# Kernel optimization log

Hardware: AMD Instinct MI355X
Metric: run time of the kernel (lower is better)

## Reference

```python
import jax, jax.numpy as jnp
import numpy as np

# GNB per-element parameters [s, beta, R, C6] indexed by atomic number Z (rows not listed stay zero)
_ROWS = {
 1:[0.2772,1.7504,3.6516,95.99], 2:[0.2425,2.087,2.1843,40.67], 3:[0.3266,2.3073,1.2711,70.21],
 4:[0.3964,2.8811,3.3497,114.51], 5:[0.3121,2.6366,2.7079,152.36], 6:[0.2455,3.0189,1.8219,184.28],
 7:[0.2743,2.9432,2.4667,482.54], 8:[0.2577,2.7407,2.365,405.57], 9:[0.2791,2.5863,1.5062,218.45],
 10:[0.2378,2.5307,1.8233,174.81], 11:[0.2592,2.5679,1.3974,181.7], 12:[0.3837,2.9613,3.3515,263.02],
 13:[0.3013,3.2377,3.0102,228.1], 14:[0.3202,3.2749,3.1629,359.43], 15:[0.3399,3.7491,3.2554,3222.12],
 16:[0.3215,3.6718,2.9539,2144.49], 17:[0.3071,3.418,3.0368,2072.46], 18:[0.2752,3.3306,2.6598,1357.42],
 19:[0.2264,2.9736,4.0877,1406.65], 20:[0.4015,3.4464,4.1275,1058.36], 21:[0.9388,4.5955,9.7282,11498.73],
 22:[0.6048,3.5334,8.5322,3361.33], 23:[0.3678,3.068,7.2344,2095.91], 24:[0.2848,2.8393,5.3605,1049.31],
 25:[0.355,3.055,3.718,966.27], 26:[0.4406,3.2628,3.6408,1571.36], 27:[0.4124,3.2622,3.4961,1183.59],
 28:[0.3139,2.749,3.5108,787.76], 29:[0.3345,2.9097,3.0537,563.93], 30:[0.3391,2.9024,3.0261,592.91],
 31:[0.3146,3.3924,3.1735,430.82], 32:[0.3327,3.2804,3.1773,812.57], 33:[0.404,3.8757,3.8357,4533.53],
 34:[0.3343,3.8562,3.1109,3440.92], 35:[0.3242,3.7067,3.2122,3859.82], 36:[0.292,3.6457,2.8263,2729.6],
 37:[0.2677,3.4421,2.412,1864.19], 38:[0.3446,3.559,1.894,1175.73], 39:[1.0038,5.7293,11.2061,32141.18],
 40:[0.6146,5.075,6.821,27655.14], 41:[0.4244,3.7156,7.2367,2864.2], 42:[0.4882,3.6853,3.901,3563.45],
 43:[0.4439,3.6987,4.0857,3266.43], 44:[0.4736,3.7826,4.045,3967.23], 45:[0.4039,3.4706,3.4813,2233.82],
 46:[0.3188,3.3433,3.0487,1393.49], 47:[0.2948,3.1186,2.7795,1315.09], 48:[0.3012,3.0853,2.8673,1311.47],
 49:[0.3351,3.5452,3.3339,1460.56], 50:[0.3134,3.2997,3.0086,1662.99], 51:[0.4081,4.1277,3.9919,8089.97],
 52:[0.3585,4.1795,3.4209,6887.05], 53:[0.3574,4.0988,3.5649,8799.32], 54:[0.3134,4.0387,3.0288,6136.5],
 55:[0.2872,3.8468,2.262,3757.31], 56:[0.3788,4.0368,1.3837,2561.18], 57:[1.0851,6.1365,12.171,66580.83],
 72:[0.5577,5.213,6.0791,27593.76], 73:[0.5308,4.7637,5.7661,15364.65], 74:[0.3926,3.6018,3.6366,2734.5],
 75:[0.5351,3.9552,4.241,4801.82], 76:[0.4701,4.0278,4.1348,5685.94], 77:[0.3661,3.6123,3.4213,2786.0],
 78:[0.3411,3.6066,3.2486,2699.79], 79:[0.3164,3.3822,2.9588,2282.6], 80:[0.3047,3.375,2.9381,2476.79],
 81:[0.2802,3.3964,2.7711,2988.7], 82:[0.2682,3.2481,2.5816,2506.63], 83:[0.3876,4.1225,3.785,8916.84],
 84:[0.3679,4.2313,3.5381,8694.22], 85:[0.368,4.2455,3.6985,11821.61], 86:[0.3195,4.1784,3.0551,8410.64],
}
_TAB = np.zeros((87, 4), np.float32)
for _z, _v in _ROWS.items():
    _TAB[_z] = _v
GNB_TABLE = jnp.asarray(_TAB)
C_SP2 = jnp.asarray(np.array([0.2808, 3.0548, 2.2348, 429.69], np.float32))
C_SP3 = jnp.asarray(np.array([0.2455, 3.0189, 1.8219, 184.28], np.float32))
N_CN2 = jnp.asarray(np.array([0.2996, 3.02, 2.6454, 720.18], np.float32))
N_CN3 = jnp.asarray(np.array([0.2743, 2.9432, 2.4667, 482.54], np.float32))

BJ_A1, BJ_A2, BJ_ALPHA = 0.4, 4.0, 14.0
CUTOFF_LR, CUTOFF_START = 10.0, 8.0  # cutoff_start = cutoff_lr - 2.0


def _poly_envelope(x):
    # PolynomialCutoff.calculate_envelope with r_max=1, p=6:
    x6 = x ** 6
    env = 1.0 - 28.0 * x6 + 48.0 * x6 * x - 21.0 * x6 * x * x
    return env * (x < 1.0)


def _gnb_forward(lengths, Z, edge_index):
    n_nodes = Z.shape[0]
    sender, receiver = edge_index[0], edge_index[1]

    # coordination numbers via scatter-add on receiver
    cn = jnp.zeros((n_nodes,), jnp.int32).at[receiver].add(1)

    # species-indexed params with CN-adaptive selection for C and N
    params = GNB_TABLE[Z]  # [N, 4]
    c_params = jnp.where((cn <= 3)[:, None], C_SP2[None, :], C_SP3[None, :])
    n_params = jnp.where((cn <= 2)[:, None], N_CN2[None, :], N_CN3[None, :])
    params = jnp.where((Z == 6)[:, None], c_params, params)
    params = jnp.where((Z == 7)[:, None], n_params, params)

    R_i = params[:, 2]
    C6_i = params[:, 3]

    # geometric-mean combination rules per edge
    C6_ij = jnp.sqrt(C6_i[sender] * C6_i[receiver])
    R_ij = jnp.sqrt(R_i[sender] * R_i[receiver])

    r = lengths
    # BJ damping: f = 1 / (1 + 6 (r/r0)^(-alpha)), r0 = a1 sqrt(R_ij) + a2
    r0 = BJ_A1 * jnp.sqrt(R_ij) + BJ_A2
    f_damp = 1.0 / (1.0 + 6.0 * (r0 / r) ** BJ_ALPHA)

    e_edge = -C6_ij / (R_ij ** 6 + r ** 6) * f_damp

    # long-range polynomial cutoff switching from 1 at cutoff_start to 0 at cutoff_lr
    x = (r - CUTOFF_START) / (CUTOFF_LR - CUTOFF_START)
    env = jnp.where(r < CUTOFF_START, 1.0, _poly_envelope(x))
    e_edge = e_edge * env

    # scatter-sum to atoms; 0.5 to split symmetric pair energy over both directions
    node_energy = jnp.zeros((n_nodes,), e_edge.dtype).at[receiver].add(0.5 * e_edge)
    return node_energy


def setup_inputs() -> dict:
    key = jax.random.key(0)
    k1, k2, k3 = jax.random.split(key, 3)
    n_nodes, n_edges = 100000, 6400000
    Z = jax.random.randint(k1, (n_nodes,), 1, 87, dtype=jnp.int32)
    edge_index = jax.random.randint(k2, (2, n_edges), 0, n_nodes, dtype=jnp.int32)
    lengths = jax.random.uniform(k3, (n_edges,), jnp.float32, 1.0, 10.5)
    return {"Z": Z, "edge_index": edge_index, "lengths": lengths}


def reference(Z, edge_index, lengths):
    return _gnb_forward(lengths, Z, edge_index)
```

## Files before the change

kernel.cpp:

```cpp
#include <hip/hip_runtime.h>


#define B2SHIFT 10
#define B2SIZE  1024
#define TILE    4096
#define SBLK    512
#define ESLICES 8
#define MAXB    128
#define EB      256
#define AREP    4

__device__ __constant__ float2 GNB_RC6[87] = {
    {0.f, 0.f},
    {3.6516f, 95.99f},   {2.1843f, 40.67f},   {1.2711f, 70.21f},
    {3.3497f, 114.51f},  {2.7079f, 152.36f},  {1.8219f, 184.28f},
    {2.4667f, 482.54f},  {2.365f, 405.57f},   {1.5062f, 218.45f},
    {1.8233f, 174.81f},  {1.3974f, 181.7f},   {3.3515f, 263.02f},
    {3.0102f, 228.1f},   {3.1629f, 359.43f},  {3.2554f, 3222.12f},
    {2.9539f, 2144.49f}, {3.0368f, 2072.46f}, {2.6598f, 1357.42f},
    {4.0877f, 1406.65f}, {4.1275f, 1058.36f}, {9.7282f, 11498.73f},
    {8.5322f, 3361.33f}, {7.2344f, 2095.91f}, {5.3605f, 1049.31f},
    {3.718f, 966.27f},   {3.6408f, 1571.36f}, {3.4961f, 1183.59f},
    {3.5108f, 787.76f},  {3.0537f, 563.93f},  {3.0261f, 592.91f},
    {3.1735f, 430.82f},  {3.1773f, 812.57f},  {3.8357f, 4533.53f},
    {3.1109f, 3440.92f}, {3.2122f, 3859.82f}, {2.8263f, 2729.6f},
    {2.412f, 1864.19f},  {1.894f, 1175.73f},  {11.2061f, 32141.18f},
    {6.821f, 27655.14f}, {7.2367f, 2864.2f},  {3.901f, 3563.45f},
    {4.0857f, 3266.43f}, {4.045f, 3967.23f},  {3.4813f, 2233.82f},
    {3.0487f, 1393.49f}, {2.7795f, 1315.09f}, {2.8673f, 1311.47f},
    {3.3339f, 1460.56f}, {3.0086f, 1662.99f}, {3.9919f, 8089.97f},
    {3.4209f, 6887.05f}, {3.5649f, 8799.32f}, {3.0288f, 6136.5f},
    {2.262f, 3757.31f},  {1.3837f, 2561.18f}, {12.171f, 66580.83f},
    {0.f,0.f},{0.f,0.f},{0.f,0.f},{0.f,0.f},{0.f,0.f},{0.f,0.f},{0.f,0.f},
    {0.f,0.f},{0.f,0.f},{0.f,0.f},{0.f,0.f},{0.f,0.f},{0.f,0.f},{0.f,0.f},
    {6.0791f, 27593.76f}, {5.7661f, 15364.65f}, {3.6366f, 2734.5f},
    {4.241f, 4801.82f},   {4.1348f, 5685.94f},  {3.4213f, 2786.0f},
    {3.2486f, 2699.79f},  {2.9588f, 2282.6f},   {2.9381f, 2476.79f},
    {2.7711f, 2988.7f},   {2.5816f, 2506.63f},  {3.785f, 8916.84f},
    {3.5381f, 8694.22f},  {3.6985f, 11821.61f}, {3.0551f, 8410.64f},
};

__global__ void gnb_init(const int* __restrict__ Z, unsigned* __restrict__ isCN,
                         int nw, int n_nodes, int4* __restrict__ zp4, int zq,
                         int* __restrict__ zp, int zwords) {
    int stride = gridDim.x * blockDim.x;
    int t0 = blockIdx.x * blockDim.x + threadIdx.x;
    int4 z4 = make_int4(0, 0, 0, 0);
    for (int i = t0; i < zq; i += stride) zp4[i] = z4;
    for (int i = zq * 4 + t0; i < zwords; i += stride) zp[i] = 0;
    for (int w = t0; w < nw; w += stride) {
        unsigned m = 0;
        int base = w << 5;
        int lim = n_nodes - base; if (lim > 32) lim = 32;
        for (int k = 0; k < lim; ++k) {
            int z = Z[base + k];
            if (z == 6 || z == 7) m |= (1u << k);
        }
        isCN[w] = m;
    }
}

__global__ void __launch_bounds__(EB)
gnb_degree(const int* __restrict__ recv, const unsigned* __restrict__ isCN,
           int* __restrict__ cn, int n_edges) {
    int base = (blockIdx.x * EB + threadIdx.x) * 4;
    if (base + 3 < n_edges) {
        int4 rv = *(const int4*)(recv + base);
        int rr[4] = {rv.x, rv.y, rv.z, rv.w};
        #pragma unroll
        for (int j = 0; j < 4; ++j) {
            unsigned r = (unsigned)rr[j];
            if ((isCN[r >> 5] >> (r & 31)) & 1u) atomicAdd(&cn[r], 1);
        }
    } else {
        for (int j = 0; j < 4; ++j) {
            int e = base + j;
            if (e < n_edges) {
                unsigned r = (unsigned)recv[e];
                if ((isCN[r >> 5] >> (r & 31)) & 1u) atomicAdd(&cn[r], 1);
            }
        }
    }
}

__global__ void gnb_params(const int* __restrict__ Z, const int* __restrict__ cn,
                           float2* __restrict__ P2, int n_nodes) {
    int i = blockIdx.x * blockDim.x + threadIdx.x;
    if (i >= n_nodes) return;
    int z = Z[i];
    float Rp, C6;
    if (z == 6) {
        if (cn[i] <= 3) { Rp = 2.2348f; C6 = 429.69f; }
        else            { Rp = 1.8219f; C6 = 184.28f; }
    } else if (z == 7) {
        if (cn[i] <= 2) { Rp = 2.6454f; C6 = 720.18f; }
        else            { Rp = 2.4667f; C6 = 482.54f; }
    } else {
        float2 rc = GNB_RC6[z];
        Rp = rc.x; C6 = rc.y;
    }
    P2[i] = make_float2(sqrtf(C6), sqrtf(sqrtf(Rp)));
}

__device__ __forceinline__ float gnb_energy_eval(float2 ps, float2 pr, float rlen) {
    float env;
    if (rlen < 8.0f) {
        env = 1.0f;
    } else {
        float x = (rlen - 8.0f) * 0.5f;
        float x2 = x * x;
        float x6 = x2 * x2 * x2;
        env = 1.0f - 28.0f * x6 + 48.0f * x6 * x - 21.0f * x6 * x2;
    }
    float sR  = ps.y * pr.y;
    float C6  = ps.x * pr.x;
    float Rij = sR * sR;
    float R3  = Rij * Rij * Rij;
    float R6  = R3 * R3;
    float r0  = 0.4f * sR + 4.0f;
    float t   = r0 / rlen;
    float t2 = t * t, t4 = t2 * t2, t8 = t4 * t4;
    float t14 = t8 * t4 * t2;
    float fd = 1.0f / (1.0f + 6.0f * t14);
    float rl2 = rlen * rlen;
    float r6 = rl2 * rl2 * rl2;
    return -0.5f * C6 / (R6 + r6) * fd * env;
}

__global__ void __launch_bounds__(SBLK)
gnb_scatter(const int* __restrict__ send, const int* __restrict__ recv,
            const float* __restrict__ len, const float2* __restrict__ P2,
            unsigned* __restrict__ buckets, unsigned* __restrict__ cursor,
            uint2* __restrict__ ovrec, unsigned* __restrict__ ocur,
            int n_edges, unsigned cap, unsigned ocap) {
    __shared__ unsigned hist[MAXB];
    __shared__ unsigned gbase[MAXB];
    const int tid = threadIdx.x;
    const int e0  = blockIdx.x * TILE;

    if (tid < MAXB) hist[tid] = 0;
    __syncthreads();

    int ss[8]; unsigned rr[8]; float ll[8];
    const bool full = (e0 + TILE <= n_edges);
    if (full) {
        int4   sv0 = *(const int4*)(send + e0 + tid * 4);
        int4   rv0 = *(const int4*)(recv + e0 + tid * 4);
        float4 lv0 = *(const float4*)(len + e0 + tid * 4);
        int4   sv1 = *(const int4*)(send + e0 + 2048 + tid * 4);
        int4   rv1 = *(const int4*)(recv + e0 + 2048 + tid * 4);
        float4 lv1 = *(const float4*)(len + e0 + 2048 + tid * 4);
        ss[0]=sv0.x; ss[1]=sv0.y; ss[2]=sv0.z; ss[3]=sv0.w;
        ss[4]=sv1.x; ss[5]=sv1.y; ss[6]=sv1.z; ss[7]=sv1.w;
        rr[0]=(unsigned)rv0.x; rr[1]=(unsigned)rv0.y; rr[2]=(unsigned)rv0.z; rr[3]=(unsigned)rv0.w;
        rr[4]=(unsigned)rv1.x; rr[5]=(unsigned)rv1.y; rr[6]=(unsigned)rv1.z; rr[7]=(unsigned)rv1.w;
        ll[0]=lv0.x; ll[1]=lv0.y; ll[2]=lv0.z; ll[3]=lv0.w;
        ll[4]=lv1.x; ll[5]=lv1.y; ll[6]=lv1.z; ll[7]=lv1.w;
    } else {
        #pragma unroll
        for (int i = 0; i < 8; ++i) {
            int e = e0 + ((i >> 2) * 2048) + tid * 4 + (i & 3);
            bool ok = (e < n_edges);
            ss[i] = ok ? send[e] : 0;
            rr[i] = ok ? (unsigned)recv[e] : 0u;
            ll[i] = ok ? len[e] : 1.0e9f;
        }
    }

    float2 Ps[8], Pr[8];
    #pragma unroll
    for (int i = 0; i < 8; ++i) { Ps[i] = P2[ss[i]]; Pr[i] = P2[rr[i]]; }

    unsigned bk[8];
    #pragma unroll
    for (int i = 0; i < 8; ++i) {
        if (ll[i] < 10.0f) {
            unsigned b   = rr[i] >> B2SHIFT;
            unsigned off = atomicAdd(&hist[b], 1u);
            bk[i] = b | ((rr[i] & (B2SIZE - 1)) << 7) | (off << 17);
        } else {
            bk[i] = 0x80000000u;
        }
    }
    __syncthreads();

    if (tid < MAXB) {
        unsigned c = hist[tid];
        gbase[tid] = c ? atomicAdd(&cursor[tid], c) : 0u;
    }
    float ev[8];
    #pragma unroll
    for (int i = 0; i < 8; ++i) ev[i] = gnb_energy_eval(Ps[i], Pr[i], ll[i]);
    __syncthreads();

    #pragma unroll
    for (int i = 0; i < 8; ++i) {
        unsigned bo = bk[i];
        if (!(bo & 0x80000000u)) {
            unsigned b    = bo & (MAXB - 1);
            unsigned rlow = (bo >> 7) & (B2SIZE - 1);
            unsigned g    = gbase[b] + (bo >> 17);
            unsigned eb   = (__float_as_uint(ev[i]) + 512u) & ~1023u;
            if (g < cap) {
                buckets[(size_t)b * cap + g] = eb | rlow;
            } else {
                unsigned o = atomicAdd(ocur, 1u);
                if (o < ocap) ovrec[o] = make_uint2((b << B2SHIFT) | rlow, eb);
            }
        }
    }
}

__global__ void __launch_bounds__(256)
gnb_accum(const unsigned* __restrict__ buckets, const unsigned* __restrict__ cursor,
          const uint2* __restrict__ ovrec, const unsigned* __restrict__ ocur,
          float* __restrict__ rep, unsigned cap, unsigned ocap) {
    __shared__ float acc[AREP][B2SIZE + 8];
    const int b   = blockIdx.x / ESLICES;
    const int sl  = blockIdx.x % ESLICES;
    const int tid = threadIdx.x;
    const int rr  = (tid >> 6) & (AREP - 1);

    for (int i = tid; i < AREP * (B2SIZE + 8); i += 256) acc[0][i] = 0.0f;
    __syncthreads();

    unsigned count = cursor[b];
    if (count > cap) count = cap;
    unsigned seg = (((count + ESLICES - 1) / ESLICES) + 3u) & ~3u;
    unsigned st  = (unsigned)sl * seg; if (st > count) st = count;
    unsigned en  = st + seg; if (en > count) en = count;

    const unsigned* src = buckets + (size_t)b * cap;
    for (unsigned i = st + tid * 4; i < en; i += 1024) {
        if (i + 4 <= en) {
            uint4 v = *(const uint4*)(src + i);
            atomicAdd(&acc[rr][v.x & (B2SIZE - 1)], __uint_as_float(v.x & ~1023u));
            atomicAdd(&acc[rr][v.y & (B2SIZE - 1)], __uint_as_float(v.y & ~1023u));
            atomicAdd(&acc[rr][v.z & (B2SIZE - 1)], __uint_as_float(v.z & ~1023u));
            atomicAdd(&acc[rr][v.w & (B2SIZE - 1)], __uint_as_float(v.w & ~1023u));
        } else {
            for (unsigned t = i; t < en; ++t) {
                unsigned v = src[t];
                atomicAdd(&acc[rr][v & (B2SIZE - 1)], __uint_as_float(v & ~1023u));
            }
        }
    }

    if (sl == 0) {
        unsigned n = *ocur; if (n > ocap) n = ocap;
        for (unsigned i = tid; i < n; i += 256) {
            uint2 rc = ovrec[i];
            if ((rc.x >> B2SHIFT) == (unsigned)b)
                atomicAdd(&acc[rr][rc.x & (B2SIZE - 1)], __uint_as_float(rc.y));
        }
    }
    __syncthreads();

    float* dst = rep + (size_t)blockIdx.x * B2SIZE;
    for (int i = tid; i < B2SIZE; i += 256)
        dst[i] = (acc[0][i] + acc[1][i]) + (acc[2][i] + acc[3][i]);
}

__global__ void gnb_reduce(const float* __restrict__ rep, float* __restrict__ out,
                           int n_nodes) {
    int i = blockIdx.x * blockDim.x + threadIdx.x;
    if (i >= n_nodes) return;
    int b = i >> B2SHIFT;
    int j = i & (B2SIZE - 1);
    const float* src = rep + ((size_t)b * ESLICES) * B2SIZE + j;
    float sum = 0.0f;
    #pragma unroll
    for (int s = 0; s < ESLICES; ++s) sum += src[(size_t)s * B2SIZE];
    out[i] = sum;
}

extern "C" void kernel_launch(void* const* d_in, const int* in_sizes, int n_in,
                              void* d_out, int out_size, void* d_ws, size_t ws_size,
                              hipStream_t stream) {
    const int*   Z    = (const int*)d_in[0];
    const int*   eidx = (const int*)d_in[1];
    const float* len  = (const float*)d_in[2];
    float*       out  = (float*)d_out;

    const int n_nodes = in_sizes[0];
    const int n_edges = in_sizes[2];
    const int* send = eidx;
    const int* recv = eidx + n_edges;

    const int NB2 = (n_nodes + B2SIZE - 1) >> B2SHIFT;
    const int nw  = (n_nodes + 31) >> 5;
    const int nwp = (nw + 7) & ~7;

    char* ws = (char*)d_ws;
    unsigned* cursor = (unsigned*)ws;
    unsigned* ocur   = (unsigned*)(ws + MAXB * 4);
    int*      cn     = (int*)(ws + (MAXB + 8) * 4);
    float2*   P2     = (float2*)(ws + ((size_t)n_nodes + MAXB + 8) * 4);
    unsigned* isCN   = (unsigned*)(ws + ((size_t)3 * n_nodes + MAXB + 8) * 4);
    float*    rep    = (float*)((char*)isCN + (size_t)nwp * 4);
    size_t rep_w     = (size_t)NB2 * ESLICES * B2SIZE;
    char*     tail   = (char*)rep + rep_w * 4;

    size_t fixed_words = (size_t)3 * n_nodes + MAXB + 8 + nwp + rep_w;
    size_t total_words = ws_size / 4;
    size_t avail = total_words > fixed_words ? total_words - fixed_words : 0;
    size_t ovw = avail / 64;
    unsigned ocap = (unsigned)((ovw / 2) & ~1ull);
    size_t capw = (avail - ovw) / (size_t)NB2;
    capw &= ~(size_t)3;
    long cap = (long)capw;
    if (cap > n_edges) cap = (n_edges + 3) & ~3;
    if (cap < 0) cap = 0;
    uint2*    ovrec   = (uint2*)tail;
    unsigned* buckets = (unsigned*)(tail + (size_t)ocap * 8);

    const int B = 256;
    int node_blocks = (n_nodes + B - 1) / B;
    int edge4_blocks = (n_edges + EB * 4 - 1) / (EB * 4);
    int scat_blocks = (n_edges + TILE - 1) / TILE;
    int zero_words  = n_nodes + MAXB + 8;
    int zq = zero_words / 4;

    gnb_init<<<256, B, 0, stream>>>(Z, isCN, nw, n_nodes, (int4*)ws, zq,
                                    (int*)ws, zero_words);
    gnb_degree<<<edge4_blocks, EB, 0, stream>>>(recv, isCN, cn, n_edges);
    gnb_params<<<node_blocks, B, 0, stream>>>(Z, cn, P2, n_nodes);
    gnb_scatter<<<scat_blocks, SBLK, 0, stream>>>(send, recv, len, P2, buckets,
                                                  cursor, ovrec, ocur, n_edges,
                                                  (unsigned)cap, ocap);
    gnb_accum<<<NB2 * ESLICES, B, 0, stream>>>(buckets, cursor, ovrec, ocur,
                                               rep, (unsigned)cap, ocap);
    gnb_reduce<<<node_blocks, B, 0, stream>>>(rep, out, n_nodes);
}
```

Before: 240.0 us.

## Fuse degree counting into scatter pass and defer energy eval to accumulation

Removes the separate degree kernel by counting carbon/nitrogen coordination inside the scatter pass, which now runs before parameter computation. Scatter buckets therefore hold raw (sender, receiver-low, length) records instead of precomputed energies, and the accumulate kernel gathers sender parameters and evaluates the energy, caching receiver parameters in shared memory. This avoids one full read of the receiver array and a separate launch, but doubles the bucket record size and so raises write and read traffic in the scatter and accumulate stages. It also moves the random sender-parameter gathers into the accumulate kernel.

Result: faster. 200.0 us (-16.7%).

```diff
diff --git a/kernel.cpp b/kernel.cpp
--- a/kernel.cpp
+++ b/kernel.cpp
@@ -7,7 +7,6 @@
 #define SBLK    512
 #define ESLICES 8
 #define MAXB    128
-#define EB      256
 #define AREP    4
 
 __device__ __constant__ float2 GNB_RC6[87] = {
@@ -60,29 +59,6 @@
     }
 }
 
-__global__ void __launch_bounds__(EB)
-gnb_degree(const int* __restrict__ recv, const unsigned* __restrict__ isCN,
-           int* __restrict__ cn, int n_edges) {
-    int base = (blockIdx.x * EB + threadIdx.x) * 4;
-    if (base + 3 < n_edges) {
-        int4 rv = *(const int4*)(recv + base);
-        int rr[4] = {rv.x, rv.y, rv.z, rv.w};
-        #pragma unroll
-        for (int j = 0; j < 4; ++j) {
-            unsigned r = (unsigned)rr[j];
-            if ((isCN[r >> 5] >> (r & 31)) & 1u) atomicAdd(&cn[r], 1);
-        }
-    } else {
-        for (int j = 0; j < 4; ++j) {
-            int e = base + j;
-            if (e < n_edges) {
-                unsigned r = (unsigned)recv[e];
-                if ((isCN[r >> 5] >> (r & 31)) & 1u) atomicAdd(&cn[r], 1);
-            }
-        }
-    }
-}
-
 __global__ void gnb_params(const int* __restrict__ Z, const int* __restrict__ cn,
                            float2* __restrict__ P2, int n_nodes) {
     int i = blockIdx.x * blockDim.x + threadIdx.x;
@@ -129,9 +105,10 @@
 
 __global__ void __launch_bounds__(SBLK)
 gnb_scatter(const int* __restrict__ send, const int* __restrict__ recv,
-            const float* __restrict__ len, const float2* __restrict__ P2,
-            unsigned* __restrict__ buckets, unsigned* __restrict__ cursor,
-            uint2* __restrict__ ovrec, unsigned* __restrict__ ocur,
+            const float* __restrict__ len, const unsigned* __restrict__ isCN,
+            int* __restrict__ cn,
+            uint2* __restrict__ buckets, unsigned* __restrict__ cursor,
+            uint4* __restrict__ ovrec, unsigned* __restrict__ ocur,
             int n_edges, unsigned cap, unsigned ocap) {
     __shared__ unsigned hist[MAXB];
     __shared__ unsigned gbase[MAXB];
@@ -141,7 +118,7 @@
     if (tid < MAXB) hist[tid] = 0;
     __syncthreads();
 
-    int ss[8]; unsigned rr[8]; float ll[8];
+    unsigned ss[8]; unsigned rr[8]; float ll[8];
     const bool full = (e0 + TILE <= n_edges);
     if (full) {
         int4   sv0 = *(const int4*)(send + e0 + tid * 4);
@@ -150,8 +127,8 @@
         int4   sv1 = *(const int4*)(send + e0 + 2048 + tid * 4);
         int4   rv1 = *(const int4*)(recv + e0 + 2048 + tid * 4);
         float4 lv1 = *(const float4*)(len + e0 + 2048 + tid * 4);
-        ss[0]=sv0.x; ss[1]=sv0.y; ss[2]=sv0.z; ss[3]=sv0.w;
-        ss[4]=sv1.x; ss[5]=sv1.y; ss[6]=sv1.z; ss[7]=sv1.w;
+        ss[0]=(unsigned)sv0.x; ss[1]=(unsigned)sv0.y; ss[2]=(unsigned)sv0.z; ss[3]=(unsigned)sv0.w;
+        ss[4]=(unsigned)sv1.x; ss[5]=(unsigned)sv1.y; ss[6]=(unsigned)sv1.z; ss[7]=(unsigned)sv1.w;
         rr[0]=(unsigned)rv0.x; rr[1]=(unsigned)rv0.y; rr[2]=(unsigned)rv0.z; rr[3]=(unsigned)rv0.w;
         rr[4]=(unsigned)rv1.x; rr[5]=(unsigned)rv1.y; rr[6]=(unsigned)rv1.z; rr[7]=(unsigned)rv1.w;
         ll[0]=lv0.x; ll[1]=lv0.y; ll[2]=lv0.z; ll[3]=lv0.w;
@@ -161,15 +138,17 @@
         for (int i = 0; i < 8; ++i) {
             int e = e0 + ((i >> 2) * 2048) + tid * 4 + (i & 3);
             bool ok = (e < n_edges);
-            ss[i] = ok ? send[e] : 0;
+            ss[i] = ok ? (unsigned)send[e] : 0u;
             rr[i] = ok ? (unsigned)recv[e] : 0u;
             ll[i] = ok ? len[e] : 1.0e9f;
         }
     }
 
-    float2 Ps[8], Pr[8];
     #pragma unroll
-    for (int i = 0; i < 8; ++i) { Ps[i] = P2[ss[i]]; Pr[i] = P2[rr[i]]; }
+    for (int i = 0; i < 8; ++i) {
+        if (ll[i] < 1.0e8f && ((isCN[rr[i] >> 5] >> (rr[i] & 31)) & 1u))
+            atomicAdd(&cn[rr[i]], 1);
+    }
 
     unsigned bk[8];
     #pragma unroll
@@ -177,7 +156,7 @@
         if (ll[i] < 10.0f) {
             unsigned b   = rr[i] >> B2SHIFT;
             unsigned off = atomicAdd(&hist[b], 1u);
-            bk[i] = b | ((rr[i] & (B2SIZE - 1)) << 7) | (off << 17);
+            bk[i] = b | (off << 7);
         } else {
             bk[i] = 0x80000000u;
         }
@@ -188,40 +167,43 @@
         unsigned c = hist[tid];
         gbase[tid] = c ? atomicAdd(&cursor[tid], c) : 0u;
     }
-    float ev[8];
-    #pragma unroll
-    for (int i = 0; i < 8; ++i) ev[i] = gnb_energy_eval(Ps[i], Pr[i], ll[i]);
     __syncthreads();
 
     #pragma unroll
     for (int i = 0; i < 8; ++i) {
         unsigned bo = bk[i];
         if (!(bo & 0x80000000u)) {
-            unsigned b    = bo & (MAXB - 1);
-            unsigned rlow = (bo >> 7) & (B2SIZE - 1);
-            unsigned g    = gbase[b] + (bo >> 17);
-            unsigned eb   = (__float_as_uint(ev[i]) + 512u) & ~1023u;
+            unsigned b = bo & (MAXB - 1);
+            unsigned g = gbase[b] + (bo >> 7);
+            unsigned x = ss[i] | ((rr[i] & (B2SIZE - 1)) << 17);
             if (g < cap) {
-                buckets[(size_t)b * cap + g] = eb | rlow;
+                buckets[(size_t)b * cap + g] = make_uint2(x, __float_as_uint(ll[i]));
             } else {
                 unsigned o = atomicAdd(ocur, 1u);
-                if (o < ocap) ovrec[o] = make_uint2((b << B2SHIFT) | rlow, eb);
+                if (o < ocap)
+                    ovrec[o] = make_uint4(rr[i], ss[i], __float_as_uint(ll[i]), 0u);
             }
         }
     }
 }
 
 __global__ void __launch_bounds__(256)
-gnb_accum(const unsigned* __restrict__ buckets, const unsigned* __restrict__ cursor,
-          const uint2* __restrict__ ovrec, const unsigned* __restrict__ ocur,
-          float* __restrict__ rep, unsigned cap, unsigned ocap) {
-    __shared__ float acc[AREP][B2SIZE + 8];
+gnb_accum(const uint2* __restrict__ buckets, const unsigned* __restrict__ cursor,
+          const uint4* __restrict__ ovrec, const unsigned* __restrict__ ocur,
+          const float2* __restrict__ P2, float* __restrict__ rep,
+          unsigned cap, unsigned ocap, int n_nodes) {
+    __shared__ float  acc[AREP][B2SIZE + 8];
+    __shared__ float2 p2loc[B2SIZE];
     const int b   = blockIdx.x / ESLICES;
     const int sl  = blockIdx.x % ESLICES;
     const int tid = threadIdx.x;
-    const int rr  = (tid >> 6) & (AREP - 1);
+    const int rp  = (tid >> 6) & (AREP - 1);
 
     for (int i = tid; i < AREP * (B2SIZE + 8); i += 256) acc[0][i] = 0.0f;
+    for (int i = tid; i < B2SIZE; i += 256) {
+        int node = (b << B2SHIFT) + i;
+        p2loc[i] = (node < n_nodes) ? P2[node] : make_float2(0.f, 0.f);
+    }
     __syncthreads();
 
     unsigned count = cursor[b];
@@ -230,18 +212,29 @@
     unsigned st  = (unsigned)sl * seg; if (st > count) st = count;
     unsigned en  = st + seg; if (en > count) en = count;
 
-    const unsigned* src = buckets + (size_t)b * cap;
+    const uint2* src = buckets + (size_t)b * cap;
     for (unsigned i = st + tid * 4; i < en; i += 1024) {
         if (i + 4 <= en) {
-            uint4 v = *(const uint4*)(src + i);
-            atomicAdd(&acc[rr][v.x & (B2SIZE - 1)], __uint_as_float(v.x & ~1023u));
-            atomicAdd(&acc[rr][v.y & (B2SIZE - 1)], __uint_as_float(v.y & ~1023u));
-            atomicAdd(&acc[rr][v.z & (B2SIZE - 1)], __uint_as_float(v.z & ~1023u));
-            atomicAdd(&acc[rr][v.w & (B2SIZE - 1)], __uint_as_float(v.w & ~1023u));
+            uint4 q0 = *(const uint4*)(src + i);
+            uint4 q1 = *(const uint4*)(src + i + 2);
+            unsigned sx[4] = {q0.x, q0.z, q1.x, q1.z};
+            unsigned lb[4] = {q0.y, q0.w, q1.y, q1.w};
+            float2 ps[4];
+            #pragma unroll
+            for (int j = 0; j < 4; ++j) ps[j] = P2[sx[j] & 0x1FFFFu];
+            #pragma unroll
+            for (int j = 0; j < 4; ++j) {
+                unsigned rlow = (sx[j] >> 17) & (B2SIZE - 1);
+                float e = gnb_energy_eval(ps[j], p2loc[rlow], __uint_as_float(lb[j]));
+                atomicAdd(&acc[rp][rlow], e);
+            }
         } else {
             for (unsigned t = i; t < en; ++t) {
-                unsigned v = src[t];
-                atomicAdd(&acc[rr][v & (B2SIZE - 1)], __uint_as_float(v & ~1023u));
+                uint2 rec = src[t];
+                unsigned rlow = (rec.x >> 17) & (B2SIZE - 1);
+                float e = gnb_energy_eval(P2[rec.x & 0x1FFFFu], p2loc[rlow],
+                                          __uint_as_float(rec.y));
+                atomicAdd(&acc[rp][rlow], e);
             }
         }
     }
@@ -249,9 +242,12 @@
     if (sl == 0) {
         unsigned n = *ocur; if (n > ocap) n = ocap;
         for (unsigned i = tid; i < n; i += 256) {
-            uint2 rc = ovrec[i];
-            if ((rc.x >> B2SHIFT) == (unsigned)b)
-                atomicAdd(&acc[rr][rc.x & (B2SIZE - 1)], __uint_as_float(rc.y));
+            uint4 rc = ovrec[i];
+            if ((rc.x >> B2SHIFT) == (unsigned)b) {
+                float e = gnb_energy_eval(P2[rc.y], p2loc[rc.x & (B2SIZE - 1)],
+                                          __uint_as_float(rc.z));
+                atomicAdd(&acc[rp][rc.x & (B2SIZE - 1)], e);
+            }
         }
     }
     __syncthreads();
@@ -305,30 +301,28 @@
     size_t total_words = ws_size / 4;
     size_t avail = total_words > fixed_words ? total_words - fixed_words : 0;
     size_t ovw = avail / 64;
-    unsigned ocap = (unsigned)((ovw / 2) & ~1ull);
+    unsigned ocap = (unsigned)(ovw / 4);
     size_t capw = (avail - ovw) / (size_t)NB2;
-    capw &= ~(size_t)3;
-    long cap = (long)capw;
+    long cap = (long)((capw / 2) & ~(size_t)3);
     if (cap > n_edges) cap = (n_edges + 3) & ~3;
     if (cap < 0) cap = 0;
-    uint2*    ovrec   = (uint2*)tail;
-    unsigned* buckets = (unsigned*)(tail + (size_t)ocap * 8);
+    uint4* ovrec   = (uint4*)tail;
+    uint2* buckets = (uint2*)(tail + (size_t)ocap * 16);
 
     const int B = 256;
     int node_blocks = (n_nodes + B - 1) / B;
-    int edge4_blocks = (n_edges + EB * 4 - 1) / (EB * 4);
     int scat_blocks = (n_edges + TILE - 1) / TILE;
     int zero_words  = n_nodes + MAXB + 8;
     int zq = zero_words / 4;
 
     gnb_init<<<256, B, 0, stream>>>(Z, isCN, nw, n_nodes, (int4*)ws, zq,
                                     (int*)ws, zero_words);
-    gnb_degree<<<edge4_blocks, EB, 0, stream>>>(recv, isCN, cn, n_edges);
+    gnb_scatter<<<scat_blocks, SBLK, 0, stream>>>(send, recv, len, isCN, cn,
+                                                  buckets, cursor, ovrec, ocur,
+                                                  n_edges, (unsigned)cap, ocap);
     gnb_params<<<node_blocks, B, 0, stream>>>(Z, cn, P2, n_nodes);
-    gnb_scatter<<<scat_blocks, SBLK, 0, stream>>>(send, recv, len, P2, buckets,
-                                                  cursor, ovrec, ocur, n_edges,
-                                                  (unsigned)cap, ocap);
     gnb_accum<<<NB2 * ESLICES, B, 0, stream>>>(buckets, cursor, ovrec, ocur,
-                                               rep, (unsigned)cap, ocap);
+                                               P2, rep, (unsigned)cap, ocap,
+                                               n_nodes);
     gnb_reduce<<<node_blocks, B, 0, stream>>>(rep, out, n_nodes);
 }
```
